# Kernel optimization log

Measured on AMD Instinct MI355X. Metric: run time of the kernel, lower is better.

The kernel has to match this reference:

```python
import jax, jax.numpy as jnp
import numpy as np

D_MODEL = 1024
NHEAD = 16
HEAD_DIM = D_MODEL // NHEAD
B, S = 8, 1024
NEG = -1e9  # finite stand-in for -inf (same softmax result, grad-safe)


def setup_inputs() -> dict:
    key = jax.random.key(0)
    ks = jax.random.split(key, 12)
    sc = 1.0 / np.sqrt(D_MODEL)
    inp = {
        "q": jax.random.normal(ks[0], (B, S, D_MODEL), jnp.float32),
        "k": jax.random.normal(ks[1], (B, S, D_MODEL), jnp.float32),
        "v": jax.random.normal(ks[2], (B, S, D_MODEL), jnp.float32),
        "padding_mask": jax.random.bernoulli(ks[3], 0.1, (B, S)),
        "causal_mask": jnp.where(jnp.tril(jnp.ones((S, S), bool)), 0.0, NEG).astype(jnp.float32),
        "wq": jax.random.normal(ks[4], (D_MODEL, D_MODEL), jnp.float32) * sc,
        "bq": jax.random.normal(ks[5], (D_MODEL,), jnp.float32) * sc,
        "wk": jax.random.normal(ks[6], (D_MODEL, D_MODEL), jnp.float32) * sc,
        "wv": jax.random.normal(ks[7], (D_MODEL, D_MODEL), jnp.float32) * sc,
        "bv": jax.random.normal(ks[8], (D_MODEL,), jnp.float32) * sc,
        "wo": jax.random.normal(ks[9], (D_MODEL, D_MODEL), jnp.float32) * sc,
        "bo": jax.random.normal(ks[10], (D_MODEL,), jnp.float32) * sc,
    }
    return inp


def reference(q, k, v, padding_mask, causal_mask, wq, bq, wk, wv, bv, wo, bo):
    b = q.shape[0]
    # projections (torch Linear: x @ W.T + b); k_linear has no bias
    qp = q @ wq.T + bq
    kp = k @ wk.T
    vp = v @ wv.T + bv
    # [B, S, H, Dh] -> [B, H, S, Dh]
    qh = qp.reshape(b, -1, NHEAD, HEAD_DIM).transpose(0, 2, 1, 3)
    kh = kp.reshape(b, -1, NHEAD, HEAD_DIM).transpose(0, 2, 1, 3)
    vh = vp.reshape(b, -1, NHEAD, HEAD_DIM).transpose(0, 2, 1, 3)
    scores = jnp.einsum("bhqd,bhkd->bhqk", qh, kh) / np.sqrt(HEAD_DIM).astype(np.float32)
    scores = jnp.where(padding_mask[:, None, None, :], NEG, scores)
    scores = scores + causal_mask[None, None, :, :]
    attn = jax.nn.softmax(scores, axis=-1)
    out = jnp.einsum("bhqk,bhkd->bhqd", attn, vh)
    out = out.transpose(0, 2, 1, 3).reshape(b, -1, D_MODEL)
    return out @ wo.T + bo
```

## Files before the change

kernel.cpp:

```cpp
#include <hip/hip_runtime.h>
#include <hip/hip_bf16.h>
#include <cstdint>
#include <math.h>


typedef __bf16 bf16_t;
typedef __bf16 bf16x8 __attribute__((ext_vector_type(8)));
typedef __bf16 bf16x4 __attribute__((ext_vector_type(4)));
typedef float  f32x4  __attribute__((ext_vector_type(4)));

#define MFMA16(a, b, c) __builtin_amdgcn_mfma_f32_16x16x32_bf16((a), (b), (c), 0, 0, 0)
#define NEGV (-1e9f)

__device__ __forceinline__ void gl_lds16(const void* gp, void* lp) {
  __builtin_amdgcn_global_load_lds(
      (__attribute__((address_space(1))) void*)(gp),
      (__attribute__((address_space(3))) void*)(lp), 16, 0, 0);
}

__device__ __forceinline__ void bar() {
  asm volatile("" ::: "memory");
  __builtin_amdgcn_s_barrier();
  asm volatile("" ::: "memory");
}

__device__ __forceinline__ unsigned int pk2(float lo, float hi) {
  unsigned short a = __builtin_bit_cast(unsigned short, (bf16_t)lo);
  unsigned short b = __builtin_bit_cast(unsigned short, (bf16_t)hi);
  return (unsigned int)a | ((unsigned int)b << 16);
}

__device__ __forceinline__ void cvt_body(const float* __restrict__ in,
                                         bf16_t* __restrict__ out, int i) {
  const float4* p = reinterpret_cast<const float4*>(in) + (size_t)i * 2;
  float4 a = p[0], b = p[1];
  bf16x8 r = {(bf16_t)a.x, (bf16_t)a.y, (bf16_t)a.z, (bf16_t)a.w,
              (bf16_t)b.x, (bf16_t)b.y, (bf16_t)b.z, (bf16_t)b.w};
  *reinterpret_cast<bf16x8*>(out + (size_t)i * 8) = r;
}

__global__ __launch_bounds__(256) void cvt_w(
    const float* __restrict__ wq, const float* __restrict__ wk,
    const float* __restrict__ wv, const float* __restrict__ wo,
    bf16_t* __restrict__ owq, bf16_t* __restrict__ owk,
    bf16_t* __restrict__ owv, bf16_t* __restrict__ owo) {
  const int bid = (int)blockIdx.x;
  const int s = bid >> 9;
  const int i = (bid & 511) * 256 + (int)threadIdx.x;
  cvt_body(s == 0 ? wq : (s == 1 ? wk : (s == 2 ? wv : wo)),
           s == 0 ? owq : (s == 1 ? owk : (s == 2 ? owv : owo)), i);
}

__global__ __launch_bounds__(256, 2) void gemm_qkv(const float* __restrict__ qf,
                                                   const float* __restrict__ kf,
                                                   const float* __restrict__ vf,
                                                   const bf16_t* __restrict__ wqb,
                                                   const bf16_t* __restrict__ wkb,
                                                   const bf16_t* __restrict__ wvb,
                                                   const float* __restrict__ bq,
                                                   const float* __restrict__ bv,
                                                   bf16_t* __restrict__ qp,
                                                   bf16_t* __restrict__ kp,
                                                   bf16_t* __restrict__ vtw) {
  __shared__ __align__(16) char lds[73728];
  const int bid = (int)blockIdx.x;
  const int z = bid >> 9;
  const int idx = bid & 511;
  const int p = ((idx >> 6) << 3) | (idx & 7);
  const int n = (idx >> 3) & 7;
  const float*  A = z == 0 ? qf : (z == 1 ? kf : vf);
  const bf16_t* W = z == 0 ? wqb : (z == 1 ? wkb : wvb);
  const int t = threadIdx.x;
  const int w = t >> 6, l = t & 63, lr = l & 15, lg = l >> 4;
  const int wr = w >> 1, wc = w & 1;
  const int m0 = p * 128, n0 = n * 128;
  const int K = 1024, N = 1024;

  const int gcA = (t & 7) ^ ((t >> 3) & 7);
  const float* Ag = A + (size_t)(m0 + (t >> 3)) * K + gcA * 4;
  const int gcB = (t & 3) ^ ((t >> 3) & 3);
  const bf16_t* Wg = W + (size_t)(n0 + (t >> 2)) * K + gcB * 8;

  auto stageA = [&](int buf, int tile) {
    char* dst = lds + buf * 16384 + t * 16;
    const size_t kt = (size_t)tile * 32;
#pragma unroll
    for (int c = 0; c < 4; c++)
      gl_lds16(Ag + (size_t)(c * 32) * K + kt, dst + c * 4096);
  };
  auto stageB = [&](int buf, int tile) {
    char* dst = lds + 49152 + buf * 8192 + t * 16;
    const size_t kt = (size_t)tile * 32;
    gl_lds16(Wg + kt,                  dst);
    gl_lds16(Wg + kt + (size_t)64 * K, dst + 4096);
  };

  stageA(0, 0); stageB(0, 0); stageA(1, 1); stageB(1, 1);
  asm volatile("s_waitcnt vmcnt(6)" ::: "memory");
  bar();

  f32x4 acc[4][4] = {};
  const int cofsB = (lg ^ ((lr >> 1) & 3)) << 4;

  for (int T = 0; T < 32; ++T) {
    const int cur = T % 3;
    const char* Ab = lds + cur * 16384;
    const char* Bb = lds + 49152 + cur * 8192;
    bf16x8 af[4], bfr[4];
#pragma unroll
    for (int mt = 0; mt < 4; mt++) {
      const int R = wr * 64 + mt * 16 + lr;
      const int sw = R & 7;
      f32x4 a0 = *(const f32x4*)(Ab + R * 128 + (((2 * lg) ^ sw) << 4));
      f32x4 a1 = *(const f32x4*)(Ab + R * 128 + (((2 * lg + 1) ^ sw) << 4));
      af[mt] = (bf16x8){(bf16_t)a0[0], (bf16_t)a0[1], (bf16_t)a0[2], (bf16_t)a0[3],
                        (bf16_t)a1[0], (bf16_t)a1[1], (bf16_t)a1[2], (bf16_t)a1[3]};
    }
#pragma unroll
    for (int nt = 0; nt < 4; nt++)
      bfr[nt] = *(const bf16x8*)(Bb + (wc * 64 + nt * 16 + lr) * 64 + cofsB);
    if (T + 2 < 32) { stageA((T + 2) % 3, T + 2); stageB((T + 2) % 3, T + 2); }
    if (T < 30)       asm volatile("s_waitcnt vmcnt(6)" ::: "memory");
    else if (T == 30) asm volatile("s_waitcnt vmcnt(0)" ::: "memory");
    bar();
    asm volatile("s_waitcnt lgkmcnt(0)" ::: "memory");
    __builtin_amdgcn_s_setprio(1);
#pragma unroll
    for (int mt = 0; mt < 4; mt++)
#pragma unroll
      for (int nt = 0; nt < 4; nt++)
        acc[mt][nt] = MFMA16(af[mt], bfr[nt], acc[mt][nt]);
    __builtin_amdgcn_s_setprio(0);
    bar();
  }

  if (z != 2) {
    bf16_t* outp = (z == 0) ? qp : kp;
    const float sc = (z == 0) ? 0.125f : 1.0f;
#pragma unroll
    for (int nt = 0; nt < 4; nt++) {
      const int col = n0 + wc * 64 + nt * 16 + lr;
      const float bb = (z == 0) ? bq[col] : 0.0f;
#pragma unroll
      for (int mt = 0; mt < 4; mt++)
#pragma unroll
        for (int i = 0; i < 4; i++) {
          const int row = m0 + wr * 64 + mt * 16 + lg * 4 + i;
          outp[(size_t)row * N + col] = (bf16_t)((acc[mt][nt][i] + bb) * sc);
        }
    }
  } else {
    __syncthreads();
    char* Tl = lds;
#pragma unroll
    for (int nt = 0; nt < 4; nt++) {
      const int col_l = wc * 64 + nt * 16 + lr;
      const float bb = bv[n0 + col_l];
#pragma unroll
      for (int mt = 0; mt < 4; mt++)
#pragma unroll
        for (int i = 0; i < 4; i++) {
          const int row_l = wr * 64 + mt * 16 + lg * 4 + i;
          *(bf16_t*)(Tl + col_l * 256 + ((row_l * 2) ^ ((col_l & 7) << 4))) =
              (bf16_t)(acc[mt][nt][i] + bb);
        }
    }
    __syncthreads();
    const int b = m0 >> 10, s0 = m0 & 1023;
    const int c_l = t >> 1, half = t & 1;
    bf16_t* dst = vtw + (size_t)(b * 1024 + n0 + c_l) * 1024 + s0 + half * 64;
    const char* Trow = Tl + c_l * 256;
    const int sw = c_l & 7;
#pragma unroll
    for (int jj = 0; jj < 8; jj++) {
      const int lc = half * 8 + jj;
      bf16x8 vv = *(const bf16x8*)(Trow + ((lc ^ sw) << 4));
      *(bf16x8*)(dst + jj * 8) = vv;
    }
  }
}

__global__ __launch_bounds__(256, 2) void gemm_out(const bf16_t* __restrict__ A,
                                                   const bf16_t* __restrict__ W,
                                                   const float* __restrict__ bias,
                                                   float* __restrict__ outp) {
  __shared__ __align__(16) char lds[49152];
  const int bid = (int)blockIdx.x;
  const int p = ((bid >> 6) << 3) | (bid & 7);
  const int n = (bid >> 3) & 7;
  const int t = threadIdx.x;
  const int w = t >> 6, l = t & 63, lr = l & 15, lg = l >> 4;
  const int wr = w >> 1, wc = w & 1;
  const int m0 = p * 128, n0 = n * 128;
  const int K = 1024, N = 1024;

  const int gc = (t & 3) ^ ((t >> 3) & 3);
  const bf16_t* Ag = A + (size_t)(m0 + (t >> 2)) * K + gc * 8;
  const bf16_t* Wg = W + (size_t)(n0 + (t >> 2)) * K + gc * 8;

  auto stageA = [&](int buf, int tile) {
    char* dst = lds + buf * 8192 + t * 16;
    const size_t kt = (size_t)tile * 32;
    gl_lds16(Ag + kt,                  dst);
    gl_lds16(Ag + kt + (size_t)64 * K, dst + 4096);
  };
  auto stageB = [&](int buf, int tile) {
    char* dst = lds + 24576 + buf * 8192 + t * 16;
    const size_t kt = (size_t)tile * 32;
    gl_lds16(Wg + kt,                  dst);
    gl_lds16(Wg + kt + (size_t)64 * K, dst + 4096);
  };

  stageA(0, 0); stageB(0, 0); stageA(1, 1); stageB(1, 1);
  asm volatile("s_waitcnt vmcnt(4)" ::: "memory");
  bar();

  f32x4 acc[4][4] = {};
  const int cofs = (lg ^ ((lr >> 1) & 3)) << 4;

  for (int T = 0; T < 32; ++T) {
    const int cur = T % 3;
    const char* Ab = lds + cur * 8192;
    const char* Bb = lds + 24576 + cur * 8192;
    bf16x8 af[4], bfr[4];
#pragma unroll
    for (int mt = 0; mt < 4; mt++)
      af[mt] = *(const bf16x8*)(Ab + (wr * 64 + mt * 16 + lr) * 64 + cofs);
#pragma unroll
    for (int nt = 0; nt < 4; nt++)
      bfr[nt] = *(const bf16x8*)(Bb + (wc * 64 + nt * 16 + lr) * 64 + cofs);
    if (T + 2 < 32) { stageA((T + 2) % 3, T + 2); stageB((T + 2) % 3, T + 2); }
    if (T < 30)       asm volatile("s_waitcnt vmcnt(4)" ::: "memory");
    else if (T == 30) asm volatile("s_waitcnt vmcnt(0)" ::: "memory");
    bar();
    asm volatile("s_waitcnt lgkmcnt(0)" ::: "memory");
    __builtin_amdgcn_s_setprio(1);
#pragma unroll
    for (int mt = 0; mt < 4; mt++)
#pragma unroll
      for (int nt = 0; nt < 4; nt++)
        acc[mt][nt] = MFMA16(af[mt], bfr[nt], acc[mt][nt]);
    __builtin_amdgcn_s_setprio(0);
    bar();
  }

#pragma unroll
  for (int nt = 0; nt < 4; nt++) {
    const int col = n0 + wc * 64 + nt * 16 + lr;
    const float bb = bias[col];
#pragma unroll
    for (int mt = 0; mt < 4; mt++)
#pragma unroll
      for (int i = 0; i < 4; i++) {
        const int row = m0 + wr * 64 + mt * 16 + lg * 4 + i;
        outp[(size_t)row * N + col] = acc[mt][nt][i] + bb;
      }
  }
}

__device__ __forceinline__ void pack_bfly(const f32x4 (&s)[4], int lg,
                                          bf16x8& pbv0, bf16x8& pbv1) {
  unsigned int u[4][2], sh[4][2];
#pragma unroll
  for (int nt = 0; nt < 4; nt++) {
    u[nt][0] = pk2(s[nt][0], s[nt][1]);
    u[nt][1] = pk2(s[nt][2], s[nt][3]);
  }
#pragma unroll
  for (int nt = 0; nt < 4; nt++) {
    sh[nt][0] = (unsigned int)__shfl_xor((int)u[nt][0], 16, 64);
    sh[nt][1] = (unsigned int)__shfl_xor((int)u[nt][1], 16, 64);
  }
  const bool ev = (lg & 1) == 0;
  unsigned int Y[8];
  Y[0] = ev ? u[0][0] : sh[1][0];  Y[1] = ev ? u[0][1] : sh[1][1];
  Y[2] = ev ? u[2][0] : sh[3][0];  Y[3] = ev ? u[2][1] : sh[3][1];
  Y[4] = ev ? sh[0][0] : u[1][0];  Y[5] = ev ? sh[0][1] : u[1][1];
  Y[6] = ev ? sh[2][0] : u[3][0];  Y[7] = ev ? sh[2][1] : u[3][1];
  const bool mid = (lg == 1) || (lg == 2);
#pragma unroll
  for (int j = 0; j < 8; j++) {
    const unsigned int z = (unsigned int)__shfl_xor((int)Y[j], 48, 64);
    Y[j] = mid ? z : Y[j];
  }
  union U8 { unsigned int u[4]; bf16x8 v; };
  U8 p0, p1;
  p0.u[0] = Y[0]; p0.u[1] = Y[1]; p0.u[2] = Y[4]; p0.u[3] = Y[5];
  p1.u[0] = Y[2]; p1.u[1] = Y[3]; p1.u[2] = Y[6]; p1.u[3] = Y[7];
  pbv0 = p0.v;
  pbv1 = p1.v;
}

__global__ __launch_bounds__(512, 8) void attn_fused(const bf16_t* __restrict__ qp,
                                                     const bf16_t* __restrict__ kp,
                                                     const bf16_t* __restrict__ vt,
                                                     const int* __restrict__ pad,
                                                     bf16_t* __restrict__ outp) {
  __shared__ bf16_t Ks[2][64 * 64];
  __shared__ bf16_t Vts[2][64 * 64];
  __shared__ int padI[1024];
  __shared__ int sfl[8], sfh[8];
  const int t = threadIdx.x, w = t >> 6, l = t & 63, lr = l & 15, lg = l >> 4;
  const int L = (int)blockIdx.x;
  const int bh = (L & 7) + ((L >> 6) << 3);
  const int j = (L >> 3) & 7;
  const int b = bh >> 4, h = bh & 15;
  const int lo = j, hi = 15 - j;

  const int srow = t >> 3, sc = t & 7;
  const int gc = sc ^ (srow & 7);
  const bf16_t* kgb = kp + (size_t)(b * 1024 + srow) * 1024 + h * 64 + gc * 8;
  const bf16_t* vgb = vt + (size_t)(bh * 64 + srow) * 1024 + gc * 8;

  auto stage = [&](int bufi, int k0s) {
    gl_lds16(kgb + (size_t)k0s * 1024, (char*)(Ks[bufi]) + t * 16);
    gl_lds16(vgb + k0s,                (char*)(Vts[bufi]) + t * 16);
  };

  bool unl = false, unh = false;
  for (int jj = t; jj <= hi * 64; jj += 512) {
    const bool u = (pad[b * 1024 + jj] == 0);
    unh |= u;
    unl |= (u && (jj <= lo * 64));
  }
  const bool al = __any(unl), ah = __any(unh);
  if (l == 0) { sfl[w] = al ? 1 : 0; sfh[w] = ah ? 1 : 0; }

  stage(0, 0);
  if (t < 256) gl_lds16(pad + b * 1024 + t * 4, (char*)padI + t * 16);

  const int mytile = (w < 4) ? hi : lo;
  const int qrow_l = mytile * 64 + (w & 3) * 16 + lr;
  const int base16 = mytile * 64 + (w & 3) * 16;
  const bf16_t* qg = qp + (size_t)(b * 1024 + qrow_l) * 1024 + h * 64 + lg * 8;
  const bf16x8 qa0 = *reinterpret_cast<const bf16x8*>(qg);
  const bf16x8 qa1 = *reinterpret_cast<const bf16x8*>(qg + 32);

  __syncthreads();
  int ul = 0, uh = 0;
#pragma unroll
  for (int i = 0; i < 8; i++) { ul |= sfl[i]; uh |= sfh[i]; }
  const bool mydeg = (w < 4) ? (uh == 0) : (ul == 0);
  const int ktEnd = (ul == 0) ? 16 : (hi + 1);

  f32x4 o[4] = {};
  float m_ = -INFINITY, ld_ = 0.0f;

  for (int kt = 0; kt < ktEnd; ++kt) {
    const int cur = kt & 1;
    if (kt + 1 < ktEnd) {
      stage(cur ^ 1, (kt + 1) * 64);
      asm volatile("s_waitcnt vmcnt(2)" ::: "memory");
    } else {
      asm volatile("s_waitcnt vmcnt(0)" ::: "memory");
    }
    __builtin_amdgcn_s_barrier();

    if (kt <= mytile || mydeg) {
      const char* Kb = (const char*)(Ks[cur]);
      const char* Vb = (const char*)(Vts[cur]);
      const int k0 = kt * 64;

      f32x4 s[4] = {};
      __builtin_amdgcn_s_setprio(1);
#pragma unroll
      for (int nt = 0; nt < 4; nt++) {
        const int row = nt * 16 + lr;
        const int sw = (row & 7) << 4;
        bf16x8 kb0 = *reinterpret_cast<const bf16x8*>(Kb + row * 128 + ((lg * 16) ^ sw));
        bf16x8 kb1 = *reinterpret_cast<const bf16x8*>(Kb + row * 128 + ((lg * 16 + 64) ^ sw));
        s[nt] = MFMA16(kb0, qa0, s[nt]);
        s[nt] = MFMA16(kb1, qa1, s[nt]);
      }
      __builtin_amdgcn_s_setprio(0);

      const bool nc = (k0 + 63 > base16);
#pragma unroll
      for (int nt = 0; nt < 4; nt++) {
        const int kc4 = k0 + nt * 16 + lg * 4;
        const int4 pd = *reinterpret_cast<const int4*>(&padI[kc4]);
        const int pdv[4] = {pd.x, pd.y, pd.z, pd.w};
#pragma unroll
        for (int i = 0; i < 4; i++) {
          float v = s[nt][i];
          if (pdv[i]) v = NEGV;
          if (nc && (kc4 + i > qrow_l)) v += NEGV;
          s[nt][i] = v;
        }
      }

      float mx = s[0][0];
#pragma unroll
      for (int nt = 0; nt < 4; nt++)
#pragma unroll
        for (int i = 0; i < 4; i++) mx = fmaxf(mx, s[nt][i]);
      mx = fmaxf(mx, __shfl_xor(mx, 16, 64));
      mx = fmaxf(mx, __shfl_xor(mx, 32, 64));

      if (!__all(mx <= m_ - 88.0f)) {
        if (!__all(mx <= m_ + 8.0f)) {
          const float mn = fmaxf(m_, mx);
          const float scl = __expf(m_ - mn);
          m_ = mn;
          ld_ *= scl;
#pragma unroll
          for (int nt = 0; nt < 4; nt++) o[nt] *= scl;
        }
        float a = 0.0f;
#pragma unroll
        for (int nt = 0; nt < 4; nt++)
#pragma unroll
          for (int i = 0; i < 4; i++) {
            const float p = __expf(s[nt][i] - m_);
            s[nt][i] = p;
            a += p;
          }
        a += __shfl_xor(a, 16, 64);
        a += __shfl_xor(a, 32, 64);
        ld_ += a;

        bf16x8 pb0, pb1;
        pack_bfly(s, lg, pb0, pb1);

        __builtin_amdgcn_s_setprio(1);
#pragma unroll
        for (int nt = 0; nt < 4; nt++) {
          const int vrow = nt * 16 + lr;
          const int vsw = (vrow & 7) << 4;
          bf16x8 vf0 = *reinterpret_cast<const bf16x8*>(Vb + vrow * 128 + ((lg * 16) ^ vsw));
          bf16x8 vf1 = *reinterpret_cast<const bf16x8*>(Vb + vrow * 128 + ((64 + lg * 16) ^ vsw));
          o[nt] = MFMA16(vf0, pb0, o[nt]);
          o[nt] = MFMA16(vf1, pb1, o[nt]);
        }
        __builtin_amdgcn_s_setprio(0);
      }
    }
    __builtin_amdgcn_s_barrier();
  }

  const float rinv = 1.0f / ld_;
#pragma unroll
  for (int nt = 0; nt < 4; nt++) {
    bf16x4 rr = {(bf16_t)(o[nt][0] * rinv), (bf16_t)(o[nt][1] * rinv),
                 (bf16_t)(o[nt][2] * rinv), (bf16_t)(o[nt][3] * rinv)};
    *reinterpret_cast<bf16x4*>(outp + (size_t)(b * 1024 + qrow_l) * 1024 + h * 64 + nt * 16 + lg * 4) = rr;
  }
}

extern "C" void kernel_launch(void* const* d_in, const int* in_sizes, int n_in,
                              void* d_out, int out_size, void* d_ws, size_t ws_size,
                              hipStream_t stream) {
  const float* q   = (const float*)d_in[0];
  const float* k   = (const float*)d_in[1];
  const float* v   = (const float*)d_in[2];
  const int*   pad = (const int*)d_in[3];
  const float* wq  = (const float*)d_in[5];
  const float* bq  = (const float*)d_in[6];
  const float* wk  = (const float*)d_in[7];
  const float* wv  = (const float*)d_in[8];
  const float* bv  = (const float*)d_in[9];
  const float* wo  = (const float*)d_in[10];
  const float* bo  = (const float*)d_in[11];

  char* ws = (char*)d_ws;
  const size_t MiB = 1024 * 1024;
  bf16_t* attnO = (bf16_t*)(ws + 0 * MiB);
  bf16_t* qp  = (bf16_t*)(ws + 48 * MiB);
  bf16_t* kp  = (bf16_t*)(ws + 64 * MiB);
  bf16_t* vtw = (bf16_t*)(ws + 80 * MiB);
  bf16_t* wqb = (bf16_t*)(ws + 96 * MiB);
  bf16_t* wkb = (bf16_t*)(ws + 98 * MiB);
  bf16_t* wvb = (bf16_t*)(ws + 100 * MiB);
  bf16_t* wob = (bf16_t*)(ws + 102 * MiB);

  cvt_w<<<2048, 256, 0, stream>>>(wq, wk, wv, wo, wqb, wkb, wvb, wob);

  gemm_qkv<<<1536, 256, 0, stream>>>(q, k, v, wqb, wkb, wvb, bq, bv, qp, kp, vtw);

  attn_fused<<<1024, 512, 0, stream>>>(qp, kp, vtw, pad, attnO);

  gemm_out<<<512, 256, 0, stream>>>(attnO, wob, bo, (float*)d_out);
}
```

Measured before the change: 167.4 us.

## Double attention key tile to 128 keys per iteration

Each loop iteration now stages and processes 128 keys instead of 64, using larger double-buffered K and V LDS tiles with a new swizzle for V. This halves the number of iterations, barriers and online-softmax rescale steps. In exchange, each block needs twice the LDS, the launch-bounds occupancy hint drops, and causal skipping becomes coarser, so more fully masked work is computed.

```diff
diff --git a/kernel.cpp b/kernel.cpp
--- a/kernel.cpp
+++ b/kernel.cpp
@@ -258,7 +258,7 @@
   }
 }
 
-__device__ __forceinline__ void pack_bfly(const f32x4 (&s)[4], int lg,
+__device__ __forceinline__ void pack_bfly(const f32x4* s, int lg,
                                           bf16x8& pbv0, bf16x8& pbv1) {
   unsigned int u[4][2], sh[4][2];
 #pragma unroll
@@ -291,13 +291,13 @@
   pbv1 = p1.v;
 }
 
-__global__ __launch_bounds__(512, 8) void attn_fused(const bf16_t* __restrict__ qp,
+__global__ __launch_bounds__(512, 4) void attn_fused(const bf16_t* __restrict__ qp,
                                                      const bf16_t* __restrict__ kp,
                                                      const bf16_t* __restrict__ vt,
                                                      const int* __restrict__ pad,
                                                      bf16_t* __restrict__ outp) {
-  __shared__ bf16_t Ks[2][64 * 64];
-  __shared__ bf16_t Vts[2][64 * 64];
+  __shared__ bf16_t Ks[2][128 * 64];
+  __shared__ bf16_t Vts[2][64 * 128];
   __shared__ int padI[1024];
   __shared__ int sfl[8], sfh[8];
   const int t = threadIdx.x, w = t >> 6, l = t & 63, lr = l & 15, lg = l >> 4;
@@ -307,14 +307,16 @@
   const int b = bh >> 4, h = bh & 15;
   const int lo = j, hi = 15 - j;
 
-  const int srow = t >> 3, sc = t & 7;
-  const int gc = sc ^ (srow & 7);
-  const bf16_t* kgb = kp + (size_t)(b * 1024 + srow) * 1024 + h * 64 + gc * 8;
-  const bf16_t* vgb = vt + (size_t)(bh * 64 + srow) * 1024 + gc * 8;
+  const int gcK = (t & 7) ^ ((t >> 3) & 7);
+  const bf16_t* kgb = kp + (size_t)(b * 1024 + (t >> 3)) * 1024 + h * 64 + gcK * 8;
+  const int gcV = (t & 15) ^ ((t >> 4) & 7);
+  const bf16_t* vgb = vt + (size_t)(bh * 64 + (t >> 4)) * 1024 + gcV * 8;
 
   auto stage = [&](int bufi, int k0s) {
-    gl_lds16(kgb + (size_t)k0s * 1024, (char*)(Ks[bufi]) + t * 16);
-    gl_lds16(vgb + k0s,                (char*)(Vts[bufi]) + t * 16);
+    gl_lds16(kgb + (size_t)k0s * 1024,        (char*)(Ks[bufi]) + t * 16);
+    gl_lds16(kgb + (size_t)(k0s + 64) * 1024, (char*)(Ks[bufi]) + 8192 + t * 16);
+    gl_lds16(vgb + k0s,                       (char*)(Vts[bufi]) + t * 16);
+    gl_lds16(vgb + k0s + (size_t)32 * 1024,   (char*)(Vts[bufi]) + 8192 + t * 16);
   };
 
   bool unl = false, unh = false;
@@ -332,6 +334,7 @@
   const int mytile = (w < 4) ? hi : lo;
   const int qrow_l = mytile * 64 + (w & 3) * 16 + lr;
   const int base16 = mytile * 64 + (w & 3) * 16;
+  const int myend = (base16 + 15) >> 7;
   const bf16_t* qg = qp + (size_t)(b * 1024 + qrow_l) * 1024 + h * 64 + lg * 8;
   const bf16x8 qa0 = *reinterpret_cast<const bf16x8*>(qg);
   const bf16x8 qa1 = *reinterpret_cast<const bf16x8*>(qg + 32);
@@ -341,7 +344,7 @@
 #pragma unroll
   for (int i = 0; i < 8; i++) { ul |= sfl[i]; uh |= sfh[i]; }
   const bool mydeg = (w < 4) ? (uh == 0) : (ul == 0);
-  const int ktEnd = (ul == 0) ? 16 : (hi + 1);
+  const int ktEnd = (ul == 0) ? 8 : ((hi + 2) >> 1);
 
   f32x4 o[4] = {};
   float m_ = -INFINITY, ld_ = 0.0f;
@@ -349,22 +352,22 @@
   for (int kt = 0; kt < ktEnd; ++kt) {
     const int cur = kt & 1;
     if (kt + 1 < ktEnd) {
-      stage(cur ^ 1, (kt + 1) * 64);
-      asm volatile("s_waitcnt vmcnt(2)" ::: "memory");
+      stage(cur ^ 1, (kt + 1) * 128);
+      asm volatile("s_waitcnt vmcnt(4)" ::: "memory");
     } else {
       asm volatile("s_waitcnt vmcnt(0)" ::: "memory");
     }
     __builtin_amdgcn_s_barrier();
 
-    if (kt <= mytile || mydeg) {
+    if (kt <= myend || mydeg) {
       const char* Kb = (const char*)(Ks[cur]);
       const char* Vb = (const char*)(Vts[cur]);
-      const int k0 = kt * 64;
-
-      f32x4 s[4] = {};
+      const int k0 = kt * 128;
+
+      f32x4 s[8] = {};
       __builtin_amdgcn_s_setprio(1);
 #pragma unroll
-      for (int nt = 0; nt < 4; nt++) {
+      for (int nt = 0; nt < 8; nt++) {
         const int row = nt * 16 + lr;
         const int sw = (row & 7) << 4;
         bf16x8 kb0 = *reinterpret_cast<const bf16x8*>(Kb + row * 128 + ((lg * 16) ^ sw));
@@ -374,9 +377,9 @@
       }
       __builtin_amdgcn_s_setprio(0);
 
-      const bool nc = (k0 + 63 > base16);
-#pragma unroll
-      for (int nt = 0; nt < 4; nt++) {
+      const bool nc = (k0 + 127 > base16);
+#pragma unroll
+      for (int nt = 0; nt < 8; nt++) {
         const int kc4 = k0 + nt * 16 + lg * 4;
         const int4 pd = *reinterpret_cast<const int4*>(&padI[kc4]);
         const int pdv[4] = {pd.x, pd.y, pd.z, pd.w};
@@ -391,7 +394,7 @@
 
       float mx = s[0][0];
 #pragma unroll
-      for (int nt = 0; nt < 4; nt++)
+      for (int nt = 0; nt < 8; nt++)
 #pragma unroll
         for (int i = 0; i < 4; i++) mx = fmaxf(mx, s[nt][i]);
       mx = fmaxf(mx, __shfl_xor(mx, 16, 64));
@@ -408,7 +411,7 @@
         }
         float a = 0.0f;
 #pragma unroll
-        for (int nt = 0; nt < 4; nt++)
+        for (int nt = 0; nt < 8; nt++)
 #pragma unroll
           for (int i = 0; i < 4; i++) {
             const float p = __expf(s[nt][i] - m_);
@@ -419,18 +422,24 @@
         a += __shfl_xor(a, 32, 64);
         ld_ += a;
 
-        bf16x8 pb0, pb1;
-        pack_bfly(s, lg, pb0, pb1);
+        bf16x8 pbA0, pbA1, pbB0, pbB1;
+        pack_bfly(&s[0], lg, pbA0, pbA1);
+        pack_bfly(&s[4], lg, pbB0, pbB1);
 
         __builtin_amdgcn_s_setprio(1);
 #pragma unroll
         for (int nt = 0; nt < 4; nt++) {
           const int vrow = nt * 16 + lr;
-          const int vsw = (vrow & 7) << 4;
-          bf16x8 vf0 = *reinterpret_cast<const bf16x8*>(Vb + vrow * 128 + ((lg * 16) ^ vsw));
-          bf16x8 vf1 = *reinterpret_cast<const bf16x8*>(Vb + vrow * 128 + ((64 + lg * 16) ^ vsw));
-          o[nt] = MFMA16(vf0, pb0, o[nt]);
-          o[nt] = MFMA16(vf1, pb1, o[nt]);
+          const int r7 = vrow & 7;
+          const char* Vr = Vb + vrow * 256;
+          bf16x8 vf00 = *reinterpret_cast<const bf16x8*>(Vr + (((0 + lg) ^ r7) << 4));
+          bf16x8 vf01 = *reinterpret_cast<const bf16x8*>(Vr + (((4 + lg) ^ r7) << 4));
+          bf16x8 vf10 = *reinterpret_cast<const bf16x8*>(Vr + 128 + (((0 + lg) ^ r7) << 4));
+          bf16x8 vf11 = *reinterpret_cast<const bf16x8*>(Vr + 128 + (((4 + lg) ^ r7) << 4));
+          o[nt] = MFMA16(vf00, pbA0, o[nt]);
+          o[nt] = MFMA16(vf01, pbA1, o[nt]);
+          o[nt] = MFMA16(vf10, pbB0, o[nt]);
+          o[nt] = MFMA16(vf11, pbB1, o[nt]);
         }
         __builtin_amdgcn_s_setprio(0);
       }
```

Result: no change. 168.5 us (+0.7%).
